# Optimization experiments

Measured on AMD Instinct MI355X. Metric: run time of the kernel, lower is better.

## Reference

```python
import jax, jax.numpy as jnp
import numpy as np

BATCH, DIM, ORDER = 16384, 1024, 3

def setup_inputs() -> dict:
    key = jax.random.key(0)
    k1, k2, k3 = jax.random.split(key, 3)
    x0 = jax.random.normal(k1, (BATCH, DIM), dtype=jnp.float32)
    # xavier-uniform init scale for w of shape (d, 1): sqrt(6/(d+1))
    limit = float(np.sqrt(6.0 / (DIM + 1)))
    W = jax.random.uniform(k2, (ORDER, DIM), dtype=jnp.float32, minval=-limit, maxval=limit)
    B = jnp.zeros((ORDER, DIM), dtype=jnp.float32)
    return {"x0": x0, "W": W, "B": B}

def reference(x0, W, B):
    # CrossLayer: xi_next = (x0 xi^T) w + b + xi == x0 * (xi . w) + b + xi
    # (outer product followed by matmul with w collapses to a dot-product scale)
    xi = x0
    for l in range(W.shape[0]):  # small fixed number of cross layers
        s = xi @ W[l]                      # [B]  dot(xi, w_l)
        xi = x0 * s[:, None] + B[l] + xi   # [B, D]
    return xi
```

## Files before the change

kernel.cpp:

```cpp
#include <hip/hip_runtime.h>


#define CN_BATCH 16384
#define CN_DIM   1024

#define WAVES_PER_BLOCK 4
#define GROUPS          4
#define GROUP_ROWS      2
#define ROWS_PER_WAVE   (GROUPS * GROUP_ROWS)
#define ROWS_PER_BLOCK  (WAVES_PER_BLOCK * ROWS_PER_WAVE)
#define GRID_BLOCKS     (CN_BATCH / ROWS_PER_BLOCK)

typedef float f32x4 __attribute__((ext_vector_type(4)));

__device__ __forceinline__ float fma4(f32x4 x, f32x4 w, float acc) {
    acc = fmaf(x.x, w.x, acc); acc = fmaf(x.y, w.y, acc);
    acc = fmaf(x.z, w.z, acc); acc = fmaf(x.w, w.w, acc);
    return acc;
}

__global__ __launch_bounds__(256, 2) void
crossnet_kernel(const float* __restrict__ x0,
                const float* __restrict__ W,
                const float* __restrict__ B,
                float* __restrict__ out)
{
    const int tid  = threadIdx.x;
    const int wave = tid >> 6;
    const int lane = tid & 63;
    const int off0 = lane * 4;

    const size_t row0 = ((size_t)blockIdx.x * WAVES_PER_BLOCK + wave) * ROWS_PER_WAVE;
    const float* __restrict__ xr = x0 + row0 * CN_DIM;

    f32x4 cur[GROUP_ROWS][4], nxt[GROUP_ROWS][4];
#pragma unroll
    for (int r = 0; r < GROUP_ROWS; ++r)
#pragma unroll
        for (int c = 0; c < 4; ++c)
            cur[r][c] = *reinterpret_cast<const f32x4*>(xr + r * CN_DIM + c * 256 + off0);

    f32x4 w0[4], w1[4], w2[4], bs[4];
    float t1 = 0.f, t2 = 0.f;
#pragma unroll
    for (int c = 0; c < 4; ++c) {
        const int off = c * 256 + off0;
        w0[c] = *reinterpret_cast<const f32x4*>(W + 0 * CN_DIM + off);
        w1[c] = *reinterpret_cast<const f32x4*>(W + 1 * CN_DIM + off);
        w2[c] = *reinterpret_cast<const f32x4*>(W + 2 * CN_DIM + off);
        const f32x4 b0 = *reinterpret_cast<const f32x4*>(B + 0 * CN_DIM + off);
        const f32x4 b1 = *reinterpret_cast<const f32x4*>(B + 1 * CN_DIM + off);
        const f32x4 b2 = *reinterpret_cast<const f32x4*>(B + 2 * CN_DIM + off);
        bs[c] = b0 + b1 + b2;
        t1 = fma4(b0, w1[c], t1);
        t2 = fma4(b0 + b1, w2[c], t2);
    }

#pragma unroll
    for (int g = 0; g < GROUPS; ++g) {
        if (g + 1 < GROUPS) {
#pragma unroll
            for (int r = 0; r < GROUP_ROWS; ++r)
#pragma unroll
                for (int c = 0; c < 4; ++c)
                    nxt[r][c] = *reinterpret_cast<const f32x4*>(
                        xr + (size_t)((g + 1) * GROUP_ROWS + r) * CN_DIM + c * 256 + off0);
        }

        float a[GROUP_ROWS][3];
#pragma unroll
        for (int r = 0; r < GROUP_ROWS; ++r) {
            a[r][0] = 0.f; a[r][1] = 0.f; a[r][2] = 0.f;
        }
#pragma unroll
        for (int c = 0; c < 4; ++c) {
#pragma unroll
            for (int r = 0; r < GROUP_ROWS; ++r) {
                a[r][0] = fma4(cur[r][c], w0[c], a[r][0]);
                a[r][1] = fma4(cur[r][c], w1[c], a[r][1]);
                a[r][2] = fma4(cur[r][c], w2[c], a[r][2]);
            }
        }

#pragma unroll
        for (int o = 1; o < 64; o <<= 1) {
#pragma unroll
            for (int r = 0; r < GROUP_ROWS; ++r) {
                a[r][0] += __shfl_xor(a[r][0], o, 64);
                a[r][1] += __shfl_xor(a[r][1], o, 64);
                a[r][2] += __shfl_xor(a[r][2], o, 64);
            }
            if (g == 0) {
                t1 += __shfl_xor(t1, o, 64);
                t2 += __shfl_xor(t2, o, 64);
            }
        }

#pragma unroll
        for (int r = 0; r < GROUP_ROWS; ++r) {
            const float s0 = a[r][0];
            const float s1 = fmaf(1.f + s0, a[r][1], t1);
            const float s2 = fmaf(1.f + s0 + s1, a[r][2], t2);
            const float cf = 1.f + s0 + s1 + s2;
            float* __restrict__ orow = out + (row0 + (size_t)(g * GROUP_ROWS + r)) * CN_DIM;
#pragma unroll
            for (int c = 0; c < 4; ++c) {
                f32x4 o;
                o.x = fmaf(cur[r][c].x, cf, bs[c].x);
                o.y = fmaf(cur[r][c].y, cf, bs[c].y);
                o.z = fmaf(cur[r][c].z, cf, bs[c].z);
                o.w = fmaf(cur[r][c].w, cf, bs[c].w);
                *reinterpret_cast<f32x4*>(orow + c * 256 + off0) = o;
            }
        }

#pragma unroll
        for (int r = 0; r < GROUP_ROWS; ++r)
#pragma unroll
            for (int c = 0; c < 4; ++c)
                cur[r][c] = nxt[r][c];
    }
}

extern "C" void kernel_launch(void* const* d_in, const int* in_sizes, int n_in,
                              void* d_out, int out_size, void* d_ws, size_t ws_size,
                              hipStream_t stream)
{
    const float* x0 = (const float*)d_in[0];
    const float* W  = (const float*)d_in[1];
    const float* B  = (const float*)d_in[2];
    float* out      = (float*)d_out;

    dim3 grid(GRID_BLOCKS);
    dim3 block(WAVES_PER_BLOCK * 64);
    crossnet_kernel<<<grid, block, 0, stream>>>(x0, W, B, out);
}
```

Baseline: 116.2 us.

## Split cross-net into a coefficient pass and a streaming scale pass

Result: slower. 122.5 us (+5.5%).

```diff
diff --git a/kernel.cpp b/kernel.cpp
--- a/kernel.cpp
+++ b/kernel.cpp
@@ -3,13 +3,6 @@
 
 #define CN_BATCH 16384
 #define CN_DIM   1024
-
-#define WAVES_PER_BLOCK 4
-#define GROUPS          4
-#define GROUP_ROWS      2
-#define ROWS_PER_WAVE   (GROUPS * GROUP_ROWS)
-#define ROWS_PER_BLOCK  (WAVES_PER_BLOCK * ROWS_PER_WAVE)
-#define GRID_BLOCKS     (CN_BATCH / ROWS_PER_BLOCK)
 
 typedef float f32x4 __attribute__((ext_vector_type(4)));
 
@@ -19,23 +12,167 @@
     return acc;
 }
 
+#define P1_WAVES       4
+#define P1_GROUPS      4
+#define P1_GROUP_ROWS  2
+#define P1_ROWS_WAVE   (P1_GROUPS * P1_GROUP_ROWS)
+#define P1_BLOCKS      (CN_BATCH / (P1_WAVES * P1_ROWS_WAVE))
+
 __global__ __launch_bounds__(256, 2) void
-crossnet_kernel(const float* __restrict__ x0,
-                const float* __restrict__ W,
-                const float* __restrict__ B,
-                float* __restrict__ out)
+crossnet_pass1(const float* __restrict__ x0, const float* __restrict__ W,
+               const float* __restrict__ B,  float* __restrict__ cf)
 {
     const int tid  = threadIdx.x;
     const int wave = tid >> 6;
     const int lane = tid & 63;
     const int off0 = lane * 4;
 
-    const size_t row0 = ((size_t)blockIdx.x * WAVES_PER_BLOCK + wave) * ROWS_PER_WAVE;
+    const size_t row0 = ((size_t)blockIdx.x * P1_WAVES + wave) * P1_ROWS_WAVE;
     const float* __restrict__ xr = x0 + row0 * CN_DIM;
 
-    f32x4 cur[GROUP_ROWS][4], nxt[GROUP_ROWS][4];
-#pragma unroll
-    for (int r = 0; r < GROUP_ROWS; ++r)
+    f32x4 cur[P1_GROUP_ROWS][4], nxt[P1_GROUP_ROWS][4];
+#pragma unroll
+    for (int r = 0; r < P1_GROUP_ROWS; ++r)
+#pragma unroll
+        for (int c = 0; c < 4; ++c)
+            cur[r][c] = *reinterpret_cast<const f32x4*>(xr + r * CN_DIM + c * 256 + off0);
+
+    f32x4 w0[4], w1[4], w2[4];
+    float t1 = 0.f, t2 = 0.f;
+#pragma unroll
+    for (int c = 0; c < 4; ++c) {
+        const int off = c * 256 + off0;
+        w0[c] = *reinterpret_cast<const f32x4*>(W + 0 * CN_DIM + off);
+        w1[c] = *reinterpret_cast<const f32x4*>(W + 1 * CN_DIM + off);
+        w2[c] = *reinterpret_cast<const f32x4*>(W + 2 * CN_DIM + off);
+        const f32x4 b0 = *reinterpret_cast<const f32x4*>(B + 0 * CN_DIM + off);
+        const f32x4 b1 = *reinterpret_cast<const f32x4*>(B + 1 * CN_DIM + off);
+        t1 = fma4(b0, w1[c], t1);
+        t2 = fma4(b0 + b1, w2[c], t2);
+    }
+
+#pragma unroll
+    for (int g = 0; g < P1_GROUPS; ++g) {
+        if (g + 1 < P1_GROUPS) {
+#pragma unroll
+            for (int r = 0; r < P1_GROUP_ROWS; ++r)
+#pragma unroll
+                for (int c = 0; c < 4; ++c)
+                    nxt[r][c] = *reinterpret_cast<const f32x4*>(
+                        xr + (size_t)((g + 1) * P1_GROUP_ROWS + r) * CN_DIM + c * 256 + off0);
+        }
+
+        float a[P1_GROUP_ROWS][3];
+#pragma unroll
+        for (int r = 0; r < P1_GROUP_ROWS; ++r) { a[r][0] = a[r][1] = a[r][2] = 0.f; }
+#pragma unroll
+        for (int c = 0; c < 4; ++c)
+#pragma unroll
+            for (int r = 0; r < P1_GROUP_ROWS; ++r) {
+                a[r][0] = fma4(cur[r][c], w0[c], a[r][0]);
+                a[r][1] = fma4(cur[r][c], w1[c], a[r][1]);
+                a[r][2] = fma4(cur[r][c], w2[c], a[r][2]);
+            }
+
+#pragma unroll
+        for (int o = 1; o < 64; o <<= 1) {
+#pragma unroll
+            for (int r = 0; r < P1_GROUP_ROWS; ++r) {
+                a[r][0] += __shfl_xor(a[r][0], o, 64);
+                a[r][1] += __shfl_xor(a[r][1], o, 64);
+                a[r][2] += __shfl_xor(a[r][2], o, 64);
+            }
+            if (g == 0) {
+                t1 += __shfl_xor(t1, o, 64);
+                t2 += __shfl_xor(t2, o, 64);
+            }
+        }
+
+        if (lane == 0) {
+#pragma unroll
+            for (int r = 0; r < P1_GROUP_ROWS; ++r) {
+                const float s0 = a[r][0];
+                const float s1 = fmaf(1.f + s0, a[r][1], t1);
+                const float s2 = fmaf(1.f + s0 + s1, a[r][2], t2);
+                cf[row0 + (size_t)(g * P1_GROUP_ROWS + r)] = 1.f + s0 + s1 + s2;
+            }
+        }
+
+#pragma unroll
+        for (int r = 0; r < P1_GROUP_ROWS; ++r)
+#pragma unroll
+            for (int c = 0; c < 4; ++c)
+                cur[r][c] = nxt[r][c];
+    }
+}
+
+#define P2_WAVES     4
+#define P2_ROWS_WAVE 2
+#define P2_BLOCKS    (CN_BATCH / (P2_WAVES * P2_ROWS_WAVE))
+
+__global__ __launch_bounds__(256, 4) void
+crossnet_pass2(const float* __restrict__ x0, const float* __restrict__ B,
+               const float* __restrict__ cf, float* __restrict__ out)
+{
+    const int tid  = threadIdx.x;
+    const int wave = tid >> 6;
+    const int lane = tid & 63;
+    const int off0 = lane * 4;
+
+    const size_t row0 = ((size_t)blockIdx.x * P2_WAVES + wave) * P2_ROWS_WAVE;
+    const float* __restrict__ xr = x0 + row0 * CN_DIM;
+
+    f32x4 xv[P2_ROWS_WAVE][4];
+#pragma unroll
+    for (int r = 0; r < P2_ROWS_WAVE; ++r)
+#pragma unroll
+        for (int c = 0; c < 4; ++c)
+            xv[r][c] = *reinterpret_cast<const f32x4*>(xr + r * CN_DIM + c * 256 + off0);
+
+    const float c0 = cf[row0];
+    const float c1 = cf[row0 + 1];
+
+    f32x4 bs[4];
+#pragma unroll
+    for (int c = 0; c < 4; ++c) {
+        const int off = c * 256 + off0;
+        const f32x4 b0 = *reinterpret_cast<const f32x4*>(B + 0 * CN_DIM + off);
+        const f32x4 b1 = *reinterpret_cast<const f32x4*>(B + 1 * CN_DIM + off);
+        const f32x4 b2 = *reinterpret_cast<const f32x4*>(B + 2 * CN_DIM + off);
+        bs[c] = b0 + b1 + b2;
+    }
+
+    const float cfr[P2_ROWS_WAVE] = { c0, c1 };
+#pragma unroll
+    for (int r = 0; r < P2_ROWS_WAVE; ++r) {
+        float* __restrict__ orow = out + (row0 + (size_t)r) * CN_DIM;
+#pragma unroll
+        for (int c = 0; c < 4; ++c) {
+            f32x4 o;
+            o.x = fmaf(xv[r][c].x, cfr[r], bs[c].x);
+            o.y = fmaf(xv[r][c].y, cfr[r], bs[c].y);
+            o.z = fmaf(xv[r][c].z, cfr[r], bs[c].z);
+            o.w = fmaf(xv[r][c].w, cfr[r], bs[c].w);
+            *reinterpret_cast<f32x4*>(orow + c * 256 + off0) = o;
+        }
+    }
+}
+
+__global__ __launch_bounds__(256, 2) void
+crossnet_single(const float* __restrict__ x0, const float* __restrict__ W,
+                const float* __restrict__ B,  float* __restrict__ out)
+{
+    const int tid  = threadIdx.x;
+    const int wave = tid >> 6;
+    const int lane = tid & 63;
+    const int off0 = lane * 4;
+
+    const size_t row0 = ((size_t)blockIdx.x * P1_WAVES + wave) * P1_ROWS_WAVE;
+    const float* __restrict__ xr = x0 + row0 * CN_DIM;
+
+    f32x4 cur[P1_GROUP_ROWS][4], nxt[P1_GROUP_ROWS][4];
+#pragma unroll
+    for (int r = 0; r < P1_GROUP_ROWS; ++r)
 #pragma unroll
         for (int c = 0; c < 4; ++c)
             cur[r][c] = *reinterpret_cast<const f32x4*>(xr + r * CN_DIM + c * 256 + off0);
@@ -57,65 +194,56 @@
     }
 
 #pragma unroll
-    for (int g = 0; g < GROUPS; ++g) {
-        if (g + 1 < GROUPS) {
-#pragma unroll
-            for (int r = 0; r < GROUP_ROWS; ++r)
+    for (int g = 0; g < P1_GROUPS; ++g) {
+        if (g + 1 < P1_GROUPS) {
+#pragma unroll
+            for (int r = 0; r < P1_GROUP_ROWS; ++r)
 #pragma unroll
                 for (int c = 0; c < 4; ++c)
                     nxt[r][c] = *reinterpret_cast<const f32x4*>(
-                        xr + (size_t)((g + 1) * GROUP_ROWS + r) * CN_DIM + c * 256 + off0);
-        }
-
-        float a[GROUP_ROWS][3];
-#pragma unroll
-        for (int r = 0; r < GROUP_ROWS; ++r) {
-            a[r][0] = 0.f; a[r][1] = 0.f; a[r][2] = 0.f;
-        }
-#pragma unroll
-        for (int c = 0; c < 4; ++c) {
-#pragma unroll
-            for (int r = 0; r < GROUP_ROWS; ++r) {
+                        xr + (size_t)((g + 1) * P1_GROUP_ROWS + r) * CN_DIM + c * 256 + off0);
+        }
+
+        float a[P1_GROUP_ROWS][3];
+#pragma unroll
+        for (int r = 0; r < P1_GROUP_ROWS; ++r) { a[r][0] = a[r][1] = a[r][2] = 0.f; }
+#pragma unroll
+        for (int c = 0; c < 4; ++c)
+#pragma unroll
+            for (int r = 0; r < P1_GROUP_ROWS; ++r) {
                 a[r][0] = fma4(cur[r][c], w0[c], a[r][0]);
                 a[r][1] = fma4(cur[r][c], w1[c], a[r][1]);
                 a[r][2] = fma4(cur[r][c], w2[c], a[r][2]);
             }
-        }
-
 #pragma unroll
         for (int o = 1; o < 64; o <<= 1) {
 #pragma unroll
-            for (int r = 0; r < GROUP_ROWS; ++r) {
+            for (int r = 0; r < P1_GROUP_ROWS; ++r) {
                 a[r][0] += __shfl_xor(a[r][0], o, 64);
                 a[r][1] += __shfl_xor(a[r][1], o, 64);
                 a[r][2] += __shfl_xor(a[r][2], o, 64);
             }
-            if (g == 0) {
-                t1 += __shfl_xor(t1, o, 64);
-                t2 += __shfl_xor(t2, o, 64);
-            }
-        }
-
-#pragma unroll
-        for (int r = 0; r < GROUP_ROWS; ++r) {
+            if (g == 0) { t1 += __shfl_xor(t1, o, 64); t2 += __shfl_xor(t2, o, 64); }
+        }
+#pragma unroll
+        for (int r = 0; r < P1_GROUP_ROWS; ++r) {
             const float s0 = a[r][0];
             const float s1 = fmaf(1.f + s0, a[r][1], t1);
             const float s2 = fmaf(1.f + s0 + s1, a[r][2], t2);
-            const float cf = 1.f + s0 + s1 + s2;
-            float* __restrict__ orow = out + (row0 + (size_t)(g * GROUP_ROWS + r)) * CN_DIM;
+            const float cfv = 1.f + s0 + s1 + s2;
+            float* __restrict__ orow = out + (row0 + (size_t)(g * P1_GROUP_ROWS + r)) * CN_DIM;
 #pragma unroll
             for (int c = 0; c < 4; ++c) {
                 f32x4 o;
-                o.x = fmaf(cur[r][c].x, cf, bs[c].x);
-                o.y = fmaf(cur[r][c].y, cf, bs[c].y);
-                o.z = fmaf(cur[r][c].z, cf, bs[c].z);
-                o.w = fmaf(cur[r][c].w, cf, bs[c].w);
+                o.x = fmaf(cur[r][c].x, cfv, bs[c].x);
+                o.y = fmaf(cur[r][c].y, cfv, bs[c].y);
+                o.z = fmaf(cur[r][c].z, cfv, bs[c].z);
+                o.w = fmaf(cur[r][c].w, cfv, bs[c].w);
                 *reinterpret_cast<f32x4*>(orow + c * 256 + off0) = o;
             }
         }
-
-#pragma unroll
-        for (int r = 0; r < GROUP_ROWS; ++r)
+#pragma unroll
+        for (int r = 0; r < P1_GROUP_ROWS; ++r)
 #pragma unroll
             for (int c = 0; c < 4; ++c)
                 cur[r][c] = nxt[r][c];
@@ -131,7 +259,11 @@
     const float* B  = (const float*)d_in[2];
     float* out      = (float*)d_out;
 
-    dim3 grid(GRID_BLOCKS);
-    dim3 block(WAVES_PER_BLOCK * 64);
-    crossnet_kernel<<<grid, block, 0, stream>>>(x0, W, B, out);
-}
+    if (d_ws != nullptr && ws_size >= (size_t)CN_BATCH * sizeof(float)) {
+        float* cf = (float*)d_ws;
+        crossnet_pass1<<<dim3(P1_BLOCKS), dim3(256), 0, stream>>>(x0, W, B, cf);
+        crossnet_pass2<<<dim3(P2_BLOCKS), dim3(256), 0, stream>>>(x0, B, cf, out);
+    } else {
+        crossnet_single<<<dim3(P1_BLOCKS), dim3(256), 0, stream>>>(x0, W, B, out);
+    }
+}
```
